# Kernel optimization log

Measured on AMD Instinct MI355X. Metric: run time of the kernel, lower is better.

## Reference

```python
import jax, jax.numpy as jnp
import numpy as np

EPS = 1e-5
NEG_SLOPE = 0.01
GROUPS = 8


def leaky(x):
    return jnp.where(x >= 0, x, NEG_SLOPE * x)


def group_norm(x, gamma, beta):
    # torchsparse GroupNorm on a single-batch sparse tensor: normalize over
    # all points and the channels within each group. x: [N, C]
    N, C = x.shape
    xg = x.reshape(N, GROUPS, C // GROUPS)
    mean = xg.mean(axis=(0, 2), keepdims=True)
    var = xg.var(axis=(0, 2), keepdims=True)
    xn = ((xg - mean) * jax.lax.rsqrt(var + EPS)).reshape(N, C)
    return xn * gamma + beta


def spconv(feats, W, in_map, out_map, n_out):
    # Rulebook gather -> per-offset GEMM -> scatter-add.
    # feats: [N_in, Cin], W: [K, Cin, Cout], in_map/out_map: [K, M]
    Cout = W.shape[-1]
    g = feats[in_map]                               # [K, M, Cin] gather
    c = jnp.einsum('kmc,kcd->kmd', g, W)            # [K, M, Cout]
    out = jnp.zeros((n_out, Cout), feats.dtype)
    return out.at[out_map.reshape(-1)].add(c.reshape(-1, Cout))


def residual_block(h, Wa, ga, ba, Wb, gb, bb, m_in, m_out, n_out):
    y = group_norm(spconv(h, Wa, m_in, m_out, n_out), ga, ba)
    y = group_norm(spconv(y, Wb, m_in, m_out, n_out), gb, bb)
    return leaky(y + h)  # identity downsample (inc==outc, stride==1)


def setup_inputs() -> dict:
    key = jax.random.key(0)
    ks = jax.random.split(key, 12)
    N_in, N_out, C = 600000, 150000, 64
    M1, M2 = 75000, 60000
    sc = 0.05
    inp = {
        'x': jax.random.normal(ks[0], (N_in, C), jnp.float32),
        'W1': jax.random.normal(ks[1], (8, C, C), jnp.float32) * sc,
        'g1': jnp.ones((C,), jnp.float32), 'b1': jnp.zeros((C,), jnp.float32),
        'Wa1': jax.random.normal(ks[2], (27, C, C), jnp.float32) * sc,
        'ga1': jnp.ones((C,), jnp.float32), 'ba1': jnp.zeros((C,), jnp.float32),
        'Wb1': jax.random.normal(ks[3], (27, C, C), jnp.float32) * sc,
        'gb1': jnp.ones((C,), jnp.float32), 'bb1': jnp.zeros((C,), jnp.float32),
        'Wa2': jax.random.normal(ks[4], (27, C, C), jnp.float32) * sc,
        'ga2': jnp.ones((C,), jnp.float32), 'ba2': jnp.zeros((C,), jnp.float32),
        'Wb2': jax.random.normal(ks[5], (27, C, C), jnp.float32) * sc,
        'gb2': jnp.ones((C,), jnp.float32), 'bb2': jnp.zeros((C,), jnp.float32),
        'm1_in': jax.random.randint(ks[6], (8, M1), 0, N_in, jnp.int32),
        'm1_out': jax.random.randint(ks[7], (8, M1), 0, N_out, jnp.int32),
        'm2_in': jax.random.randint(ks[8], (27, M2), 0, N_out, jnp.int32),
        'm2_out': jax.random.randint(ks[9], (27, M2), 0, N_out, jnp.int32),
        'n_out': N_out,
    }
    return inp


def reference(x, W1, g1, b1, Wa1, ga1, ba1, Wb1, gb1, bb1,
              Wa2, ga2, ba2, Wb2, gb2, bb2,
              m1_in, m1_out, m2_in, m2_out, n_out):
    # BasicConvolutionBlock: Conv3d(ks=2, stride=2) -> GroupNorm(8) -> LeakyReLU
    h = leaky(group_norm(spconv(x, W1, m1_in, m1_out, n_out), g1, b1))
    # ResidualBlock x2: (Conv3d ks=3 -> GN -> Conv3d ks=3 -> GN) + identity, LeakyReLU
    h = residual_block(h, Wa1, ga1, ba1, Wb1, gb1, bb1, m2_in, m2_out, n_out)
    h = residual_block(h, Wa2, ga2, ba2, Wb2, gb2, bb2, m2_in, m2_out, n_out)
    return h
```

## Files before the change

kernel.cpp:

```cpp
#include <hip/hip_runtime.h>

#define NEG_SLOPE 0.01f
#define GN_EPS 1e-5f

typedef __attribute__((ext_vector_type(8))) __bf16 bf16x8;
typedef __attribute__((ext_vector_type(4))) __bf16 bf16x4;
typedef __attribute__((ext_vector_type(4))) float f32x4;

__device__ __forceinline__ float bf_lo(unsigned v) { return __uint_as_float(v << 16); }
__device__ __forceinline__ float bf_hi(unsigned v) { return __uint_as_float(v & 0xffff0000u); }

__global__ __launch_bounds__(256) void hist_kernel(
    const int* __restrict__ om, int* __restrict__ cnt, int E)
{
    const int stride = gridDim.x * blockDim.x;
    for (int e = blockIdx.x * blockDim.x + threadIdx.x; e < E; e += stride)
        atomicAdd(&cnt[om[e]], 1);
}

__global__ __launch_bounds__(256) void scan1_kernel(
    const int* __restrict__ cnt, int* __restrict__ part, int N)
{
    __shared__ int ls[256];
    int b = blockIdx.x, t = threadIdx.x;
    int i0 = b * 1024 + t * 4, s = 0;
#pragma unroll
    for (int u = 0; u < 4; ++u) if (i0 + u < N) s += cnt[i0 + u];
    ls[t] = s; __syncthreads();
    for (int off = 128; off > 0; off >>= 1) {
        if (t < off) ls[t] += ls[t + off];
        __syncthreads();
    }
    if (t == 0) part[b] = ls[0];
}

__global__ void scan2_kernel(int* __restrict__ part, int nb)
{
    if (blockIdx.x == 0 && threadIdx.x == 0) {
        int run = 0;
        for (int i = 0; i < nb; ++i) { int v = part[i]; part[i] = run; run += v; }
    }
}

__global__ __launch_bounds__(256) void scan3_kernel(
    const int* __restrict__ cnt, const int* __restrict__ part,
    int* __restrict__ base, int N)
{
    __shared__ int ls[256];
    int b = blockIdx.x, t = threadIdx.x;
    int i0 = b * 1024 + t * 4;
    int v0 = 0, v1 = 0, v2 = 0, v3 = 0;
    if (i0 + 0 < N) v0 = cnt[i0 + 0];
    if (i0 + 1 < N) v1 = cnt[i0 + 1];
    if (i0 + 2 < N) v2 = cnt[i0 + 2];
    if (i0 + 3 < N) v3 = cnt[i0 + 3];
    int s = v0 + v1 + v2 + v3;
    ls[t] = s; __syncthreads();
    for (int off = 1; off < 256; off <<= 1) {
        int x = (t >= off) ? ls[t - off] : 0;
        __syncthreads();
        ls[t] += x;
        __syncthreads();
    }
    int run = part[b] + ls[t] - s;
    if (i0 + 0 < N) { base[i0 + 0] = run; run += v0; if (i0 + 0 == N - 1) base[N] = run; }
    if (i0 + 1 < N) { base[i0 + 1] = run; run += v1; if (i0 + 1 == N - 1) base[N] = run; }
    if (i0 + 2 < N) { base[i0 + 2] = run; run += v2; if (i0 + 2 == N - 1) base[N] = run; }
    if (i0 + 3 < N) { base[i0 + 3] = run; run += v3; if (i0 + 3 == N - 1) base[N] = run; }
}

__global__ __launch_bounds__(256) void scatter_kernel(
    const int* __restrict__ om, const int* __restrict__ base,
    int* __restrict__ cur, int* __restrict__ inv, int E)
{
    const int stride = gridDim.x * blockDim.x;
    for (int e = blockIdx.x * blockDim.x + threadIdx.x; e < E; e += stride) {
        int o = om[e];
        int p = base[o] + atomicAdd(&cur[o], 1);
        inv[e] = p;
    }
}

template<int F32IN>
__global__ __launch_bounds__(256) void conv_mfma_kernel(
    const void* __restrict__ feats, const float* __restrict__ W,
    const int* __restrict__ in_map, const int* __restrict__ inv,
    __bf16* __restrict__ C, int M, int BPK)
{
    const int lane = threadIdx.x & 63;
    const int wv   = threadIdx.x >> 6;
    const int k    = blockIdx.x / BPK;
    const int blk  = blockIdx.x % BPK;
    const int l15  = lane & 15;
    const int lg   = lane >> 4;

    const float* Wk = W + (size_t)k * 4096;
    bf16x8 b[4][2];
#pragma unroll
    for (int nt = 0; nt < 4; ++nt)
#pragma unroll
        for (int h = 0; h < 2; ++h)
#pragma unroll
            for (int j = 0; j < 8; ++j)
                b[nt][h][j] = (__bf16)Wk[(h * 32 + lg * 8 + j) * 64 + nt * 16 + l15];

    const int* imk   = in_map + (size_t)k * M;
    const int ntiles = (M + 15) >> 4;
    const int wpk    = BPK * 4;

    for (int t = blk * 4 + wv; t < ntiles; t += wpk) {
        int m  = t * 16 + l15;
        int mc = m < M ? m : M - 1;
        int ii = imk[mc];
        bf16x8 a0, a1;
        if (F32IN) {
            const float4* rp = (const float4*)((const float*)feats + (size_t)ii * 64 + lg * 8);
            float4 u0 = rp[0], u1 = rp[1];
            float4 u2 = rp[8], u3 = rp[9];
            a0[0] = (__bf16)u0.x; a0[1] = (__bf16)u0.y; a0[2] = (__bf16)u0.z; a0[3] = (__bf16)u0.w;
            a0[4] = (__bf16)u1.x; a0[5] = (__bf16)u1.y; a0[6] = (__bf16)u1.z; a0[7] = (__bf16)u1.w;
            a1[0] = (__bf16)u2.x; a1[1] = (__bf16)u2.y; a1[2] = (__bf16)u2.z; a1[3] = (__bf16)u2.w;
            a1[4] = (__bf16)u3.x; a1[5] = (__bf16)u3.y; a1[6] = (__bf16)u3.z; a1[7] = (__bf16)u3.w;
        } else {
            const bf16x8* rp = (const bf16x8*)((const __bf16*)feats + (size_t)ii * 64 + lg * 8);
            a0 = rp[0];
            a1 = rp[4];
        }
        f32x4 c0 = {0.f,0.f,0.f,0.f}, c1 = c0, c2 = c0, c3 = c0;
        c0 = __builtin_amdgcn_mfma_f32_16x16x32_bf16(a0, b[0][0], c0, 0, 0, 0);
        c1 = __builtin_amdgcn_mfma_f32_16x16x32_bf16(a0, b[1][0], c1, 0, 0, 0);
        c2 = __builtin_amdgcn_mfma_f32_16x16x32_bf16(a0, b[2][0], c2, 0, 0, 0);
        c3 = __builtin_amdgcn_mfma_f32_16x16x32_bf16(a0, b[3][0], c3, 0, 0, 0);
        c0 = __builtin_amdgcn_mfma_f32_16x16x32_bf16(a1, b[0][1], c0, 0, 0, 0);
        c1 = __builtin_amdgcn_mfma_f32_16x16x32_bf16(a1, b[1][1], c1, 0, 0, 0);
        c2 = __builtin_amdgcn_mfma_f32_16x16x32_bf16(a1, b[2][1], c2, 0, 0, 0);
        c3 = __builtin_amdgcn_mfma_f32_16x16x32_bf16(a1, b[3][1], c3, 0, 0, 0);

        const int e_base = k * M + t * 16;
        f32x4 cc[4] = {c0, c1, c2, c3};
#pragma unroll
        for (int r = 0; r < 4; ++r) {
            int row = lg * 4 + r;
            if (t * 16 + row < M) {
                int p = inv[e_base + row];
                __bf16* cr = C + (size_t)p * 64 + l15;
#pragma unroll
                for (int nt = 0; nt < 4; ++nt) {
                    __bf16 v = (__bf16)cc[nt][r];
                    __builtin_nontemporal_store(v, cr + nt * 16);
                }
            }
        }
    }
}

__global__ __launch_bounds__(256) void reduce_kernel(
    const unsigned short* __restrict__ C, const int* __restrict__ base,
    float* __restrict__ out, float* __restrict__ stats, int N)
{
    const int lane = threadIdx.x & 63;
    const int wv   = threadIdx.x >> 6;
    const int c2   = lane & 31;
    const int half = lane >> 5;
    float rs = 0.f, rq = 0.f;

    const int ostride = gridDim.x * 4;
    for (int o = blockIdx.x * 4 + wv; o < N; o += ostride) {
        const int s = base[o], t = base[o + 1];
        float s0 = 0.f, s1 = 0.f;
        for (int i = s + half; i < t; i += 2) {
            unsigned v = __builtin_nontemporal_load(
                (const unsigned*)(C + (size_t)i * 64 + c2 * 2));
            s0 += bf_lo(v);
            s1 += bf_hi(v);
        }
        s0 += __shfl_xor(s0, 32);
        s1 += __shfl_xor(s1, 32);
        if (half == 0) {
            float2 r = {s0, s1};
            *(float2*)(out + (size_t)o * 64 + c2 * 2) = r;
            rs += s0 + s1;
            rq += s0 * s0 + s1 * s1;
        }
    }
    rs += __shfl_xor(rs, 1); rq += __shfl_xor(rq, 1);
    rs += __shfl_xor(rs, 2); rq += __shfl_xor(rq, 2);
    __shared__ float ls[4][16];
    const int g = c2 >> 2;
    if (half == 0 && (c2 & 3) == 0) { ls[wv][g] = rs; ls[wv][8 + g] = rq; }
    __syncthreads();
    if (threadIdx.x < 16) {
        float t = (ls[0][threadIdx.x] + ls[1][threadIdx.x]) +
                  (ls[2][threadIdx.x] + ls[3][threadIdx.x]);
        unsafeAtomicAdd(stats + threadIdx.x, t);
    }
}

__global__ __launch_bounds__(256) void conv_kernel(
    const float* __restrict__ feats, const float* __restrict__ W,
    const int* __restrict__ in_map, const int* __restrict__ out_map,
    float* __restrict__ out, int M, int BPK)
{
    const int lane = threadIdx.x & 63;
    const int wv   = threadIdx.x >> 6;
    const int k    = blockIdx.x / BPK;
    const int blk  = blockIdx.x % BPK;
    const float* Wk = W + (size_t)k * 4096;
    float w[64];
#pragma unroll
    for (int c = 0; c < 64; ++c) w[c] = Wk[c * 64 + lane];
    __shared__ float fbuf[4][64];
    const int* im = in_map + (size_t)k * M;
    const int* om = out_map + (size_t)k * M;
    const int stride = BPK * 4;
    for (int m = blk * 4 + wv; m < M; m += stride) {
        int ii = im[m];
        int oi = om[m];
        float f = feats[(size_t)ii * 64 + lane];
        fbuf[wv][lane] = f;
        const float* fb = fbuf[wv];
        float a0 = 0.f, a1 = 0.f, a2 = 0.f, a3 = 0.f;
#pragma unroll
        for (int c = 0; c < 64; c += 4) {
            float4 f4 = *(const float4*)(fb + c);
            a0 = fmaf(f4.x, w[c + 0], a0);
            a1 = fmaf(f4.y, w[c + 1], a1);
            a2 = fmaf(f4.z, w[c + 2], a2);
            a3 = fmaf(f4.w, w[c + 3], a3);
        }
        unsafeAtomicAdd(out + (size_t)oi * 64 + lane, (a0 + a1) + (a2 + a3));
    }
}

__global__ __launch_bounds__(256) void gn_stats_kernel(
    const float4* __restrict__ x, float* __restrict__ stats, long total4)
{
    const int lane = threadIdx.x & 63;
    float s = 0.f, q = 0.f;
    const long stride = (long)gridDim.x * blockDim.x;
    for (long i = (long)blockIdx.x * blockDim.x + threadIdx.x; i < total4; i += stride) {
        float4 v = x[i];
        s += (v.x + v.y) + (v.z + v.w);
        q += (v.x * v.x + v.y * v.y) + (v.z * v.z + v.w * v.w);
    }
    s += __shfl_xor(s, 1);  q += __shfl_xor(q, 1);
    s += __shfl_xor(s, 16); q += __shfl_xor(q, 16);
    s += __shfl_xor(s, 32); q += __shfl_xor(q, 32);
    __shared__ float ls[4][16];
    const int wv = threadIdx.x >> 6;
    const int g = (lane >> 1) & 7;
    if (lane < 16 && (lane & 1) == 0) { ls[wv][g] = s; ls[wv][8 + g] = q; }
    __syncthreads();
    if (threadIdx.x < 16) {
        float t = (ls[0][threadIdx.x] + ls[1][threadIdx.x]) +
                  (ls[2][threadIdx.x] + ls[3][threadIdx.x]);
        unsafeAtomicAdd(stats + threadIdx.x, t);
    }
}

__global__ __launch_bounds__(256) void gn_apply_kernel(
    const float4* __restrict__ x, const float* __restrict__ stats,
    const float* __restrict__ gamma, const float* __restrict__ beta,
    const float4* resid, float4* out_f, bf16x4* out_bf,
    long total4, float invc, int do_leaky)
{
    __shared__ float sc[64], sh[64];
    if (threadIdx.x < 64) {
        int c = threadIdx.x, g = c >> 3;
        float mean = stats[g] * invc;
        float var  = fmaf(-mean, mean, stats[8 + g] * invc);
        float s    = rsqrtf(var + GN_EPS) * gamma[c];
        sc[c] = s;
        sh[c] = fmaf(-mean, s, beta[c]);
    }
    __syncthreads();
    const long stride = (long)gridDim.x * blockDim.x;
    for (long i = (long)blockIdx.x * blockDim.x + threadIdx.x; i < total4; i += stride) {
        float4 v = x[i];
        int c0 = ((int)(i & 15)) << 2;
        float4 r;
        r.x = fmaf(v.x, sc[c0 + 0], sh[c0 + 0]);
        r.y = fmaf(v.y, sc[c0 + 1], sh[c0 + 1]);
        r.z = fmaf(v.z, sc[c0 + 2], sh[c0 + 2]);
        r.w = fmaf(v.w, sc[c0 + 3], sh[c0 + 3]);
        if (resid) {
            float4 h4 = resid[i];
            r.x += h4.x; r.y += h4.y; r.z += h4.z; r.w += h4.w;
        }
        if (do_leaky) {
            r.x = r.x >= 0.f ? r.x : NEG_SLOPE * r.x;
            r.y = r.y >= 0.f ? r.y : NEG_SLOPE * r.y;
            r.z = r.z >= 0.f ? r.z : NEG_SLOPE * r.z;
            r.w = r.w >= 0.f ? r.w : NEG_SLOPE * r.w;
        }
        if (out_f) out_f[i] = r;
        if (out_bf) {
            bf16x4 o;
            o.x = (__bf16)r.x; o.y = (__bf16)r.y; o.z = (__bf16)r.z; o.w = (__bf16)r.w;
            out_bf[i] = o;
        }
    }
}

extern "C" void kernel_launch(void* const* d_in, const int* in_sizes, int n_in,
                              void* d_out, int out_size, void* d_ws, size_t ws_size,
                              hipStream_t stream) {
    const float* x   = (const float*)d_in[0];
    const float* W1  = (const float*)d_in[1];
    const float* g1  = (const float*)d_in[2];
    const float* b1  = (const float*)d_in[3];
    const float* Wa1 = (const float*)d_in[4];
    const float* ga1 = (const float*)d_in[5];
    const float* ba1 = (const float*)d_in[6];
    const float* Wb1 = (const float*)d_in[7];
    const float* gb1 = (const float*)d_in[8];
    const float* bb1 = (const float*)d_in[9];
    const float* Wa2 = (const float*)d_in[10];
    const float* ga2 = (const float*)d_in[11];
    const float* ba2 = (const float*)d_in[12];
    const float* Wb2 = (const float*)d_in[13];
    const float* gb2 = (const float*)d_in[14];
    const float* bb2 = (const float*)d_in[15];
    const int* m1_in  = (const int*)d_in[16];
    const int* m1_out = (const int*)d_in[17];
    const int* m2_in  = (const int*)d_in[18];
    const int* m2_out = (const int*)d_in[19];

    const int N   = out_size / 64;
    const int M1  = in_sizes[16] / 8;
    const int M2  = in_sizes[18] / 27;
    const int E1  = 8 * M1;
    const int E2  = 27 * M2;
    const int Emax = E1 > E2 ? E1 : E2;

    float* h = (float*)d_out;
    const long  total4 = (long)N * 16;
    const float invc   = 1.f / ((float)N * 8.f);

    char* wp = (char*)d_ws;
    size_t off = 0;
    auto alloc = [&](size_t bytes) {
        void* p = wp + off;
        off = (off + bytes + 255) & ~(size_t)255;
        return p;
    };
    float*  acc   = (float*)alloc((size_t)N * 64 * 4);
    __bf16* hbf   = (__bf16*)alloc((size_t)N * 64 * 2);
    __bf16* ybf   = (__bf16*)alloc((size_t)N * 64 * 2);
    __bf16* Cbuf  = (__bf16*)alloc((size_t)Emax * 64 * 2);
    int*    base1 = (int*)alloc((size_t)(N + 1) * 4);
    int*    base2 = (int*)alloc((size_t)(N + 1) * 4);
    int*    cnt   = (int*)alloc((size_t)N * 4);
    int*    part  = (int*)alloc(4096);
    int*    inv1  = (int*)alloc((size_t)E1 * 4);
    int*    inv2  = (int*)alloc((size_t)E2 * 4);
    float*  stats = (float*)alloc(64);
    const size_t need = off;

    if (ws_size < need) {
        float* y  = acc + (size_t)N * 64;
        float* st = y + (size_t)N * 64;
        const size_t nbytes = (size_t)N * 64 * 4;
        auto convL = [&](const float* feats, const float* W, const int* im,
                         const int* om, int K, int M, int BPK) {
            hipMemsetAsync(acc, 0, nbytes, stream);
            conv_kernel<<<dim3(K * BPK), 256, 0, stream>>>(feats, W, im, om, acc, M, BPK);
        };
        auto gnL = [&](const float* gamma, const float* beta, const float* resid,
                       float* outp, int leaky) {
            hipMemsetAsync(st, 0, 16 * sizeof(float), stream);
            gn_stats_kernel<<<1024, 256, 0, stream>>>((const float4*)acc, st, total4);
            gn_apply_kernel<<<1024, 256, 0, stream>>>((const float4*)acc, st, gamma, beta,
                                                      (const float4*)resid, (float4*)outp,
                                                      nullptr, total4, invc, leaky);
        };
        convL(x, W1, m1_in, m1_out, 8, M1, 320); gnL(g1, b1, nullptr, h, 1);
        convL(h, Wa1, m2_in, m2_out, 27, M2, 96); gnL(ga1, ba1, nullptr, y, 0);
        convL(y, Wb1, m2_in, m2_out, 27, M2, 96); gnL(gb1, bb1, h, h, 1);
        convL(h, Wa2, m2_in, m2_out, 27, M2, 96); gnL(ga2, ba2, nullptr, y, 0);
        convL(y, Wb2, m2_in, m2_out, 27, M2, 96); gnL(gb2, bb2, h, h, 1);
        return;
    }

    const int nb = (N + 1023) / 1024;
    auto buildCSR = [&](const int* om, int E, int* base, int* inv) {
        hipMemsetAsync(cnt, 0, (size_t)N * 4, stream);
        hist_kernel<<<2048, 256, 0, stream>>>(om, cnt, E);
        scan1_kernel<<<nb, 256, 0, stream>>>(cnt, part, N);
        scan2_kernel<<<1, 64, 0, stream>>>(part, nb);
        scan3_kernel<<<nb, 256, 0, stream>>>(cnt, part, base, N);
        hipMemsetAsync(cnt, 0, (size_t)N * 4, stream);
        scatter_kernel<<<2048, 256, 0, stream>>>(om, base, cnt, inv, E);
    };
    buildCSR(m1_out, E1, base1, inv1);
    buildCSR(m2_out, E2, base2, inv2);

    auto conv = [&](const void* feats, int f32in, const float* W, const int* im,
                    int K, int M, int BPK, const int* base, const int* inv) {
        hipMemsetAsync(stats, 0, 64, stream);
        if (f32in)
            conv_mfma_kernel<1><<<dim3(K * BPK), 256, 0, stream>>>(feats, W, im, inv, Cbuf, M, BPK);
        else
            conv_mfma_kernel<0><<<dim3(K * BPK), 256, 0, stream>>>(feats, W, im, inv, Cbuf, M, BPK);
        reduce_kernel<<<2048, 256, 0, stream>>>((const unsigned short*)Cbuf, base,
                                                acc, stats, N);
    };
    auto gn = [&](const float* gamma, const float* beta, const float* resid,
                  float* outf, __bf16* outbf, int leaky) {
        gn_apply_kernel<<<1024, 256, 0, stream>>>((const float4*)acc, stats, gamma, beta,
                                                  (const float4*)resid, (float4*)outf,
                                                  (bf16x4*)outbf, total4, invc, leaky);
    };

    conv(x, 1, W1, m1_in, 8, M1, 128, base1, inv1);
    gn(g1, b1, nullptr, h, hbf, 1);
    conv(hbf, 0, Wa1, m2_in, 27, M2, 64, base2, inv2);
    gn(ga1, ba1, nullptr, nullptr, ybf, 0);
    conv(ybf, 0, Wb1, m2_in, 27, M2, 64, base2, inv2);
    gn(gb1, bb1, h, h, hbf, 1);
    conv(hbf, 0, Wa2, m2_in, 27, M2, 64, base2, inv2);
    gn(ga2, ba2, nullptr, nullptr, ybf, 0);
    conv(ybf, 0, Wb2, m2_in, 27, M2, 64, base2, inv2);
    gn(gb2, bb2, h, h, hbf, 1);
}
```

Measured before the change: 1.173 ms.

## Fuse first GroupNorm of residual blocks into next conv gather; widen reduce loads

The non-leaky GroupNorm after the first conv of each residual block is no longer a separate pass. The second conv now gathers raw fp32 accumulator rows and applies the per-channel scale and shift computed from stats before converting to bf16. This removes two gn_apply launches and the bf16 intermediate write. In exchange the gather reads fp32 rows, twice the bytes of bf16, per rulebook entry.

The reduce kernel now processes four rows at a time, with 8-byte loads per lane. Stats buffers are split per layer and zeroed once up front. The final GN skips the unused bf16 output.

```diff
diff --git a/kernel.cpp b/kernel.cpp
--- a/kernel.cpp
+++ b/kernel.cpp
@@ -6,6 +6,7 @@
 typedef __attribute__((ext_vector_type(8))) __bf16 bf16x8;
 typedef __attribute__((ext_vector_type(4))) __bf16 bf16x4;
 typedef __attribute__((ext_vector_type(4))) float f32x4;
+typedef __attribute__((ext_vector_type(2))) unsigned uintx2;
 
 __device__ __forceinline__ float bf_lo(unsigned v) { return __uint_as_float(v << 16); }
 __device__ __forceinline__ float bf_hi(unsigned v) { return __uint_as_float(v & 0xffff0000u); }
@@ -81,11 +82,13 @@
     }
 }
 
-template<int F32IN>
+template<int F32IN, int NORM>
 __global__ __launch_bounds__(256) void conv_mfma_kernel(
     const void* __restrict__ feats, const float* __restrict__ W,
     const int* __restrict__ in_map, const int* __restrict__ inv,
-    __bf16* __restrict__ C, int M, int BPK)
+    __bf16* __restrict__ C, int M, int BPK,
+    const float* __restrict__ stats, const float* __restrict__ gamma,
+    const float* __restrict__ beta, float invc)
 {
     const int lane = threadIdx.x & 63;
     const int wv   = threadIdx.x >> 6;
@@ -93,6 +96,24 @@
     const int blk  = blockIdx.x % BPK;
     const int l15  = lane & 15;
     const int lg   = lane >> 4;
+
+    float scv[2][8], shv[2][8];
+    if (NORM) {
+#pragma unroll
+        for (int hh = 0; hh < 2; ++hh) {
+            int g = hh * 4 + lg;
+            float mean = stats[g] * invc;
+            float var  = fmaf(-mean, mean, stats[8 + g] * invc);
+            float rstd = rsqrtf(var + GN_EPS);
+#pragma unroll
+            for (int j = 0; j < 8; ++j) {
+                int ch = hh * 32 + lg * 8 + j;
+                float s = rstd * gamma[ch];
+                scv[hh][j] = s;
+                shv[hh][j] = fmaf(-mean, s, beta[ch]);
+            }
+        }
+    }
 
     const float* Wk = W + (size_t)k * 4096;
     bf16x8 b[4][2];
@@ -117,10 +138,18 @@
             const float4* rp = (const float4*)((const float*)feats + (size_t)ii * 64 + lg * 8);
             float4 u0 = rp[0], u1 = rp[1];
             float4 u2 = rp[8], u3 = rp[9];
-            a0[0] = (__bf16)u0.x; a0[1] = (__bf16)u0.y; a0[2] = (__bf16)u0.z; a0[3] = (__bf16)u0.w;
-            a0[4] = (__bf16)u1.x; a0[5] = (__bf16)u1.y; a0[6] = (__bf16)u1.z; a0[7] = (__bf16)u1.w;
-            a1[0] = (__bf16)u2.x; a1[1] = (__bf16)u2.y; a1[2] = (__bf16)u2.z; a1[3] = (__bf16)u2.w;
-            a1[4] = (__bf16)u3.x; a1[5] = (__bf16)u3.y; a1[6] = (__bf16)u3.z; a1[7] = (__bf16)u3.w;
+            float lo[8] = {u0.x, u0.y, u0.z, u0.w, u1.x, u1.y, u1.z, u1.w};
+            float hi[8] = {u2.x, u2.y, u2.z, u2.w, u3.x, u3.y, u3.z, u3.w};
+#pragma unroll
+            for (int j = 0; j < 8; ++j) {
+                float v0 = lo[j], v1 = hi[j];
+                if (NORM) {
+                    v0 = fmaf(v0, scv[0][j], shv[0][j]);
+                    v1 = fmaf(v1, scv[1][j], shv[1][j]);
+                }
+                a0[j] = (__bf16)v0;
+                a1[j] = (__bf16)v1;
+            }
         } else {
             const bf16x8* rp = (const bf16x8*)((const __bf16*)feats + (size_t)ii * 64 + lg * 8);
             a0 = rp[0];
@@ -155,39 +184,42 @@
 }
 
 __global__ __launch_bounds__(256) void reduce_kernel(
-    const unsigned short* __restrict__ C, const int* __restrict__ base,
+    const unsigned* __restrict__ C2, const int* __restrict__ base,
     float* __restrict__ out, float* __restrict__ stats, int N)
 {
     const int lane = threadIdx.x & 63;
     const int wv   = threadIdx.x >> 6;
-    const int c2   = lane & 31;
-    const int half = lane >> 5;
-    float rs = 0.f, rq = 0.f;
+    const int rq   = lane >> 4;
+    const int cq   = lane & 15;
+    float rs = 0.f, rqsum = 0.f;
 
     const int ostride = gridDim.x * 4;
     for (int o = blockIdx.x * 4 + wv; o < N; o += ostride) {
         const int s = base[o], t = base[o + 1];
-        float s0 = 0.f, s1 = 0.f;
-        for (int i = s + half; i < t; i += 2) {
-            unsigned v = __builtin_nontemporal_load(
-                (const unsigned*)(C + (size_t)i * 64 + c2 * 2));
-            s0 += bf_lo(v);
-            s1 += bf_hi(v);
-        }
-        s0 += __shfl_xor(s0, 32);
-        s1 += __shfl_xor(s1, 32);
-        if (half == 0) {
-            float2 r = {s0, s1};
-            *(float2*)(out + (size_t)o * 64 + c2 * 2) = r;
-            rs += s0 + s1;
-            rq += s0 * s0 + s1 * s1;
-        }
-    }
-    rs += __shfl_xor(rs, 1); rq += __shfl_xor(rq, 1);
-    rs += __shfl_xor(rs, 2); rq += __shfl_xor(rq, 2);
+        float a0 = 0.f, a1 = 0.f, a2 = 0.f, a3 = 0.f;
+        for (int i = s + rq; i < t; i += 4) {
+            uintx2 v = __builtin_nontemporal_load(
+                (const uintx2*)(C2 + (size_t)i * 32 + cq * 2));
+            a0 += bf_lo(v.x); a1 += bf_hi(v.x);
+            a2 += bf_lo(v.y); a3 += bf_hi(v.y);
+        }
+        a0 += __shfl_xor(a0, 16); a1 += __shfl_xor(a1, 16);
+        a2 += __shfl_xor(a2, 16); a3 += __shfl_xor(a3, 16);
+        a0 += __shfl_xor(a0, 32); a1 += __shfl_xor(a1, 32);
+        a2 += __shfl_xor(a2, 32); a3 += __shfl_xor(a3, 32);
+        if (rq == 0) {
+            float4 r = {a0, a1, a2, a3};
+            *(float4*)(out + (size_t)o * 64 + cq * 4) = r;
+            rs    += (a0 + a1) + (a2 + a3);
+            rqsum += (a0 * a0 + a1 * a1) + (a2 * a2 + a3 * a3);
+        }
+    }
+    rs += __shfl_xor(rs, 1); rqsum += __shfl_xor(rqsum, 1);
     __shared__ float ls[4][16];
-    const int g = c2 >> 2;
-    if (half == 0 && (c2 & 3) == 0) { ls[wv][g] = rs; ls[wv][8 + g] = rq; }
+    if (rq == 0 && (cq & 1) == 0) {
+        ls[wv][cq >> 1] = rs;
+        ls[wv][8 + (cq >> 1)] = rqsum;
+    }
     __syncthreads();
     if (threadIdx.x < 16) {
         float t = (ls[0][threadIdx.x] + ls[1][threadIdx.x]) +
@@ -344,9 +376,9 @@
         off = (off + bytes + 255) & ~(size_t)255;
         return p;
     };
-    float*  acc   = (float*)alloc((size_t)N * 64 * 4);
+    float*  accA  = (float*)alloc((size_t)N * 64 * 4);
+    float*  accB  = (float*)alloc((size_t)N * 64 * 4);
     __bf16* hbf   = (__bf16*)alloc((size_t)N * 64 * 2);
-    __bf16* ybf   = (__bf16*)alloc((size_t)N * 64 * 2);
     __bf16* Cbuf  = (__bf16*)alloc((size_t)Emax * 64 * 2);
     int*    base1 = (int*)alloc((size_t)(N + 1) * 4);
     int*    base2 = (int*)alloc((size_t)(N + 1) * 4);
@@ -354,23 +386,23 @@
     int*    part  = (int*)alloc(4096);
     int*    inv1  = (int*)alloc((size_t)E1 * 4);
     int*    inv2  = (int*)alloc((size_t)E2 * 4);
-    float*  stats = (float*)alloc(64);
+    float*  stats = (float*)alloc(5 * 16 * 4);
     const size_t need = off;
 
     if (ws_size < need) {
-        float* y  = acc + (size_t)N * 64;
-        float* st = y + (size_t)N * 64;
+        float* y  = accB;
+        float* st = stats;
         const size_t nbytes = (size_t)N * 64 * 4;
         auto convL = [&](const float* feats, const float* W, const int* im,
                          const int* om, int K, int M, int BPK) {
-            hipMemsetAsync(acc, 0, nbytes, stream);
-            conv_kernel<<<dim3(K * BPK), 256, 0, stream>>>(feats, W, im, om, acc, M, BPK);
+            hipMemsetAsync(accA, 0, nbytes, stream);
+            conv_kernel<<<dim3(K * BPK), 256, 0, stream>>>(feats, W, im, om, accA, M, BPK);
         };
         auto gnL = [&](const float* gamma, const float* beta, const float* resid,
                        float* outp, int leaky) {
             hipMemsetAsync(st, 0, 16 * sizeof(float), stream);
-            gn_stats_kernel<<<1024, 256, 0, stream>>>((const float4*)acc, st, total4);
-            gn_apply_kernel<<<1024, 256, 0, stream>>>((const float4*)acc, st, gamma, beta,
+            gn_stats_kernel<<<1024, 256, 0, stream>>>((const float4*)accA, st, total4);
+            gn_apply_kernel<<<1024, 256, 0, stream>>>((const float4*)accA, st, gamma, beta,
                                                       (const float4*)resid, (float4*)outp,
                                                       nullptr, total4, invc, leaky);
         };
@@ -381,6 +413,8 @@
         convL(y, Wb2, m2_in, m2_out, 27, M2, 96); gnL(gb2, bb2, h, h, 1);
         return;
     }
+
+    hipMemsetAsync(stats, 0, 5 * 16 * sizeof(float), stream);
 
     const int nb = (N + 1023) / 1024;
     auto buildCSR = [&](const int* om, int E, int* base, int* inv) {
@@ -395,31 +429,43 @@
     buildCSR(m1_out, E1, base1, inv1);
     buildCSR(m2_out, E2, base2, inv2);
 
-    auto conv = [&](const void* feats, int f32in, const float* W, const int* im,
-                    int K, int M, int BPK, const int* base, const int* inv) {
-        hipMemsetAsync(stats, 0, 64, stream);
-        if (f32in)
-            conv_mfma_kernel<1><<<dim3(K * BPK), 256, 0, stream>>>(feats, W, im, inv, Cbuf, M, BPK);
+    float* st0  = stats;
+    float* stA1 = stats + 16;
+    float* stB1 = stats + 32;
+    float* stA2 = stats + 48;
+    float* stB2 = stats + 64;
+
+    auto conv = [&](const void* feats, int variant, const float* W, const int* im,
+                    int K, int M, int BPK, const int* base, const int* inv,
+                    float* accOut, float* statOut,
+                    const float* nstats, const float* ngamma, const float* nbeta) {
+        dim3 grid(K * BPK);
+        if (variant == 2)
+            conv_mfma_kernel<1, 1><<<grid, 256, 0, stream>>>(feats, W, im, inv, Cbuf,
+                M, BPK, nstats, ngamma, nbeta, invc);
+        else if (variant == 1)
+            conv_mfma_kernel<1, 0><<<grid, 256, 0, stream>>>(feats, W, im, inv, Cbuf,
+                M, BPK, nullptr, nullptr, nullptr, invc);
         else
-            conv_mfma_kernel<0><<<dim3(K * BPK), 256, 0, stream>>>(feats, W, im, inv, Cbuf, M, BPK);
-        reduce_kernel<<<2048, 256, 0, stream>>>((const unsigned short*)Cbuf, base,
-                                                acc, stats, N);
+            conv_mfma_kernel<0, 0><<<grid, 256, 0, stream>>>(feats, W, im, inv, Cbuf,
+                M, BPK, nullptr, nullptr, nullptr, invc);
+        reduce_kernel<<<2048, 256, 0, stream>>>((const unsigned*)Cbuf, base,
+                                                accOut, statOut, N);
     };
-    auto gn = [&](const float* gamma, const float* beta, const float* resid,
-                  float* outf, __bf16* outbf, int leaky) {
-        gn_apply_kernel<<<1024, 256, 0, stream>>>((const float4*)acc, stats, gamma, beta,
+    auto gn = [&](const float* src, const float* st, const float* gamma,
+                  const float* beta, const float* resid, float* outf,
+                  __bf16* outbf, int leaky) {
+        gn_apply_kernel<<<1024, 256, 0, stream>>>((const float4*)src, st, gamma, beta,
                                                   (const float4*)resid, (float4*)outf,
                                                   (bf16x4*)outbf, total4, invc, leaky);
     };
 
-    conv(x, 1, W1, m1_in, 8, M1, 128, base1, inv1);
-    gn(g1, b1, nullptr, h, hbf, 1);
-    conv(hbf, 0, Wa1, m2_in, 27, M2, 64, base2, inv2);
-    gn(ga1, ba1, nullptr, nullptr, ybf, 0);
-    conv(ybf, 0, Wb1, m2_in, 27, M2, 64, base2, inv2);
-    gn(gb1, bb1, h, h, hbf, 1);
-    conv(hbf, 0, Wa2, m2_in, 27, M2, 64, base2, inv2);
-    gn(ga2, ba2, nullptr, nullptr, ybf, 0);
-    conv(ybf, 0, Wb2, m2_in, 27, M2, 64, base2, inv2);
-    gn(gb2, bb2, h, h, hbf, 1);
-}
+    conv(x, 1, W1, m1_in, 8, M1, 128, base1, inv1, accA, st0, nullptr, nullptr, nullptr);
+    gn(accA, st0, g1, b1, nullptr, h, hbf, 1);
+    conv(hbf, 0, Wa1, m2_in, 27, M2, 64, base2, inv2, accA, stA1, nullptr, nullptr, nullptr);
+    conv(accA, 2, Wb1, m2_in, 27, M2, 64, base2, inv2, accB, stB1, stA1, ga1, ba1);
+    gn(accB, stB1, gb1, bb1, h, h, hbf, 1);
+    conv(hbf, 0, Wa2, m2_in, 27, M2, 64, base2, inv2, accA, stA2, nullptr, nullptr, nullptr);
+    conv(accA, 2, Wb2, m2_in, 27, M2, 64, base2, inv2, accB, stB2, stA2, ga2, ba2);
+    gn(accB, stB2, gb2, bb2, h, h, nullptr, 1);
+}
```

Result: no change. 1.174 ms (+0.1%).
